# Performance work log

Measured on AMD Instinct MI355X. Metric: run time of the kernel, lower is better.

Reference implementation:

```python
import jax, jax.numpy as jnp
import numpy as np
import math

B, S, D, H, PD = 2, 2048, 1024, 16, 3
DK = D // H          # 64
SP = S // H          # 128, required so physics_scores matches scores shape


def setup_inputs() -> dict:
    key = jax.random.key(0)
    ks = jax.random.split(key, 16)
    sc = 0.02
    return {
        "query": jax.random.normal(ks[0], (B, S, D), jnp.float32),
        "key_in": jax.random.normal(ks[1], (B, S, D), jnp.float32),
        "value": jax.random.normal(ks[2], (B, S, D), jnp.float32),
        "physics_info": jax.random.normal(ks[3], (B, SP, PD), jnp.float32),
        "Wq": jax.random.normal(ks[4], (D, D), jnp.float32) * sc,
        "bq": jnp.zeros((D,), jnp.float32),
        "Wk": jax.random.normal(ks[5], (D, D), jnp.float32) * sc,
        "bk": jnp.zeros((D,), jnp.float32),
        "Wv": jax.random.normal(ks[6], (D, D), jnp.float32) * sc,
        "bv": jnp.zeros((D,), jnp.float32),
        "Wo": jax.random.normal(ks[7], (D, D), jnp.float32) * sc,
        "bo": jnp.zeros((D,), jnp.float32),
        "Pw": jax.random.normal(ks[8], (PD, D), jnp.float32),   # physics_weight
        "pb": jnp.zeros((1,), jnp.float32),                      # physics_bias
    }


def reference(query, key_in, value, physics_info, Wq, bq, Wk, bk, Wv, bv, Wo, bo, Pw, pb):
    b, s, d = query.shape
    inv = 1.0 / math.sqrt(DK)
    # project and split heads -> [B, H, S, DK]
    Q = (query @ Wq + bq).reshape(b, s, H, DK).transpose(0, 2, 1, 3)
    K = (key_in @ Wk + bk).reshape(b, s, H, DK).transpose(0, 2, 1, 3)
    V = (value @ Wv + bv).reshape(b, s, H, DK).transpose(0, 2, 1, 3)
    scores = jnp.einsum('bhqd,bhkd->bhqk', Q, K) * inv  # [B,H,S,S]
    # physics constraint: [B,SP,D] -> (expand over heads is a no-op) -> [B,SP*H,DK]
    pc = (physics_info @ Pw).reshape(b, SP * H, DK)
    physics_scores = jnp.einsum('bhqd,bkd->bhqk', Q, pc) * inv  # [B,H,S,S]
    scores = scores + pb[0] * physics_scores
    attn = jax.nn.softmax(scores, axis=-1)  # dropout in eval mode (identity)
    ctx = jnp.einsum('bhqk,bhkd->bhqd', attn, V)
    ctx = ctx.transpose(0, 2, 1, 3).reshape(b, s, d)
    return ctx @ Wo + bo
```

## Files before the change

### kernel.cpp

```cpp
#include <hip/hip_runtime.h>
#include <hip/hip_bf16.h>
#include <stdint.h>

typedef __bf16 bf16_t;
typedef __attribute__((ext_vector_type(8))) __bf16 bf16x8;
typedef __attribute__((ext_vector_type(4))) __bf16 bf16x4;
typedef __attribute__((ext_vector_type(4))) short short4_t;
typedef __attribute__((ext_vector_type(4))) float f32x4;

#define B_ 2
#define S_ 2048
#define D_ 1024
#define H_ 16
#define DK_ 64
#define SP_ 128

static __device__ inline f32x4 mfma16x16x16bf16(short4_t a, short4_t b, f32x4 c) {
#if __has_builtin(__builtin_amdgcn_mfma_f32_16x16x16bf16_1k)
    return __builtin_amdgcn_mfma_f32_16x16x16bf16_1k(a, b, c, 0, 0, 0);
#else
    asm volatile("v_mfma_f32_16x16x16_bf16 %0, %1, %2, %0" : "+v"(c) : "v"(a), "v"(b));
    return c;
#endif
}

__global__ __launch_bounds__(256) void physics_pc(const float* __restrict__ phys,
                                                  const float* __restrict__ Pw,
                                                  float* __restrict__ PP) {
    int i = blockIdx.x * 256 + threadIdx.x;
    int n = i & (D_ - 1);
    int sb = i >> 10;
    float acc = 0.f;
#pragma unroll
    for (int p = 0; p < 3; ++p)
        acc += phys[sb * 3 + p] * Pw[p * D_ + n];
    PP[i] = acc;
}

struct WPtrs { const float* w[4]; bf16_t* o[4]; };

__global__ __launch_bounds__(256) void wconv_t(WPtrs p) {
    __shared__ bf16_t t[32][33];
    int z = blockIdx.z;
    const float* W = p.w[z];
    bf16_t* Wt = p.o[z];
    int bx = blockIdx.x * 32, by = blockIdx.y * 32;
    int x = threadIdx.x, y0 = threadIdx.y;
#pragma unroll
    for (int j = 0; j < 32; j += 8)
        t[y0 + j][x] = (bf16_t)W[(size_t)(by + y0 + j) * D_ + bx + x];
    __syncthreads();
#pragma unroll
    for (int j = 0; j < 32; j += 8)
        Wt[(size_t)(bx + y0 + j) * D_ + by + x] = t[x][y0 + j];
}

__global__ __launch_bounds__(256) void qkv_gemm(
    const float* __restrict__ q_in, const float* __restrict__ k_in,
    const float* __restrict__ v_in,
    const bf16_t* __restrict__ WqT, const bf16_t* __restrict__ WkT,
    const bf16_t* __restrict__ WvT,
    const float* __restrict__ bq, const float* __restrict__ bk,
    const float* __restrict__ bv,
    bf16_t* __restrict__ Qo, bf16_t* __restrict__ Ko, bf16_t* __restrict__ Vo,
    const float* __restrict__ PP, const float* __restrict__ pbp) {
    __shared__ alignas(16) bf16_t lA[128 * 64];
    __shared__ alignas(16) bf16_t lB[128 * 64];
    int z = blockIdx.z;
    const float* A = (z == 0) ? q_in : (z == 1) ? k_in : v_in;
    const bf16_t* Bt = (z == 0) ? WqT : (z == 1) ? WkT : WvT;
    const float* bias = (z == 0) ? bq : (z == 1) ? bk : bv;

    int tid = threadIdx.x;
    int lane = tid & 63, wid = tid >> 6;
    int quad = lane >> 4, l15 = lane & 15;
    int bm = blockIdx.x * 128;
    int bn = blockIdx.y * 128;
    int wm = (wid >> 1) * 64, wn = (wid & 1) * 64;
    f32x4 acc[4][4] = {};

    for (int k0 = 0; k0 < D_; k0 += 64) {
        const float* gA = A + (size_t)bm * D_ + k0;
        const char* gB = (const char*)(Bt + (size_t)bn * D_ + k0);
        f32x4 a0[4], a1[4];
        bf16x8 vb[4];
#pragma unroll
        for (int j = 0; j < 4; ++j) {
            int flatB = j * 8192 + tid * 32;
            int row = flatB >> 8;
            int col = (flatB & 255) >> 2;
            const float* pA = gA + (size_t)row * D_ + col;
            a0[j] = *(const f32x4*)pA;
            a1[j] = *(const f32x4*)(pA + 4);
            int flat = j * 4096 + tid * 16;
            vb[j] = *(const bf16x8*)(gB + (size_t)(flat >> 7) * (D_ * 2) + (flat & 127));
        }
        __syncthreads();
#pragma unroll
        for (int j = 0; j < 4; ++j) {
            bf16x8 av;
#pragma unroll
            for (int e = 0; e < 4; ++e) { av[e] = (bf16_t)a0[j][e]; av[4 + e] = (bf16_t)a1[j][e]; }
            int flat = j * 4096 + tid * 16;
            *(bf16x8*)((char*)lA + flat) = av;
            *(bf16x8*)((char*)lB + flat) = vb[j];
        }
        __syncthreads();
#pragma unroll
        for (int ks = 0; ks < 2; ++ks) {
            bf16x8 af[4], bfr[4];
#pragma unroll
            for (int i = 0; i < 4; ++i) {
                af[i] = *(const bf16x8*)((const char*)lA + (wm + i * 16 + l15) * 128 + ks * 64 + quad * 16);
                bfr[i] = *(const bf16x8*)((const char*)lB + (wn + i * 16 + l15) * 128 + ks * 64 + quad * 16);
            }
#pragma unroll
            for (int i = 0; i < 4; ++i)
#pragma unroll
                for (int j = 0; j < 4; ++j)
                    acc[i][j] = __builtin_amdgcn_mfma_f32_16x16x32_bf16(af[i], bfr[j], acc[i][j], 0, 0, 0);
        }
    }

    float pb0 = (z == 1) ? pbp[0] : 0.f;
#pragma unroll
    for (int i = 0; i < 4; ++i)
#pragma unroll
        for (int j = 0; j < 4; ++j) {
            int r0 = bm + wm + i * 16 + quad * 4;
            int c = bn + wn + j * 16 + l15;
            float bv_ = bias[c];
#pragma unroll
            for (int reg = 0; reg < 4; ++reg) {
                int r = r0 + reg;
                float v = acc[i][j][reg] + bv_;
                if (z == 0) {
                    Qo[(size_t)r * D_ + c] = (bf16_t)(v * 0.125f);
                } else if (z == 1) {
                    int b = r >> 11, s = r & (S_ - 1);
                    v += pb0 * PP[((size_t)(b * SP_ + (s >> 4)) << 10) + ((s & 15) << 6) + (c & 63)];
                    Ko[(size_t)r * D_ + c] = (bf16_t)v;
                } else {
                    int b = r >> 11, s = r & (S_ - 1);
                    Vo[(((size_t)b << 10) + c) * S_ + s] = (bf16_t)v;
                }
            }
        }
}

#define KSTR 144
#define VSTR 272

__global__ __launch_bounds__(256) void flash_attn(const bf16_t* Qb,
                                                  const bf16_t* __restrict__ Kb,
                                                  const bf16_t* __restrict__ Vt,
                                                  bf16_t* Ctx) {
    __shared__ alignas(16) char lK[128 * KSTR];
    __shared__ alignas(16) char lV[64 * VSTR];
    int tid = threadIdx.x, lane = tid & 63, wid = tid >> 6;
    int quad = lane >> 4, l15 = lane & 15;
    int q0 = blockIdx.x * 128;
    int h = blockIdx.y, b = blockIdx.z;
    const bf16_t* Qh = Qb + ((size_t)b * S_) * D_ + h * DK_;
    const bf16_t* Kh = Kb + ((size_t)b * S_) * D_ + h * DK_;
    const bf16_t* Vh = Vt + ((size_t)b * D_ + h * DK_) * S_;

    {
        const char* g = (const char*)(Qh + (size_t)q0 * D_);
#pragma unroll
        for (int j = 0; j < 4; ++j) {
            int flat = j * 4096 + tid * 16;
            bf16x8 v = *(const bf16x8*)(g + (size_t)(flat >> 7) * (D_ * 2) + (flat & 127));
            *(bf16x8*)(lK + (flat >> 7) * KSTR + (flat & 127)) = v;
        }
    }
    __syncthreads();
    bf16x8 qf[2][2];
#pragma unroll
    for (int mt = 0; mt < 2; ++mt)
#pragma unroll
        for (int ks = 0; ks < 2; ++ks)
            qf[mt][ks] = *(const bf16x8*)(lK + (wid * 32 + mt * 16 + l15) * KSTR + ks * 64 + quad * 16);

    f32x4 ot[4][2] = {};
    float m_i[2], l_i[2];
#pragma unroll
    for (int mt = 0; mt < 2; ++mt) { m_i[mt] = -1e30f; l_i[mt] = 0.f; }

    for (int t = 0; t < S_ / 128; ++t) {
        const char* gK = (const char*)(Kh + (size_t)t * 128 * D_);
        const char* gV = (const char*)(Vh + (size_t)t * 128);
        bf16x8 vk[4], vv[4];
#pragma unroll
        for (int j = 0; j < 4; ++j) {
            int flat = j * 4096 + tid * 16;
            vk[j] = *(const bf16x8*)(gK + (size_t)(flat >> 7) * (D_ * 2) + (flat & 127));
            vv[j] = *(const bf16x8*)(gV + (size_t)(flat >> 8) * (S_ * 2) + (flat & 255));
        }
        __syncthreads();
#pragma unroll
        for (int j = 0; j < 4; ++j) {
            int flat = j * 4096 + tid * 16;
            *(bf16x8*)(lK + (flat >> 7) * KSTR + (flat & 127)) = vk[j];
            *(bf16x8*)(lV + (flat >> 8) * VSTR + (flat & 255)) = vv[j];
        }
        __syncthreads();

        f32x4 sc[8][2];
#pragma unroll
        for (int kt = 0; kt < 8; ++kt)
#pragma unroll
            for (int mt = 0; mt < 2; ++mt) sc[kt][mt] = (f32x4){0.f, 0.f, 0.f, 0.f};
#pragma unroll
        for (int kt = 0; kt < 8; ++kt) {
            bf16x8 kf0 = *(const bf16x8*)(lK + (kt * 16 + l15) * KSTR + quad * 16);
            bf16x8 kf1 = *(const bf16x8*)(lK + (kt * 16 + l15) * KSTR + 64 + quad * 16);
#pragma unroll
            for (int mt = 0; mt < 2; ++mt) {
                sc[kt][mt] = __builtin_amdgcn_mfma_f32_16x16x32_bf16(kf0, qf[mt][0], sc[kt][mt], 0, 0, 0);
                sc[kt][mt] = __builtin_amdgcn_mfma_f32_16x16x32_bf16(kf1, qf[mt][1], sc[kt][mt], 0, 0, 0);
            }
        }

#pragma unroll
        for (int mt = 0; mt < 2; ++mt) {
            float mloc = -1e30f;
#pragma unroll
            for (int kt = 0; kt < 8; ++kt)
#pragma unroll
                for (int r = 0; r < 4; ++r) mloc = fmaxf(mloc, sc[kt][mt][r]);
            mloc = fmaxf(mloc, __shfl_xor(mloc, 16, 64));
            mloc = fmaxf(mloc, __shfl_xor(mloc, 32, 64));
            float mnew = fmaxf(m_i[mt], mloc);
            float alpha = __expf(m_i[mt] - mnew);
            float rsum = 0.f;
#pragma unroll
            for (int kt = 0; kt < 8; ++kt)
#pragma unroll
                for (int r = 0; r < 4; ++r) {
                    float p = __expf(sc[kt][mt][r] - mnew);
                    sc[kt][mt][r] = p;
                    rsum += p;
                }
            rsum += __shfl_xor(rsum, 16, 64);
            rsum += __shfl_xor(rsum, 32, 64);
            l_i[mt] = l_i[mt] * alpha + rsum;
            m_i[mt] = mnew;
#pragma unroll
            for (int dt = 0; dt < 4; ++dt)
#pragma unroll
                for (int r = 0; r < 4; ++r) ot[dt][mt][r] *= alpha;
        }

#pragma unroll
        for (int kt = 0; kt < 8; ++kt) {
            short4_t bp[2];
#pragma unroll
            for (int mt = 0; mt < 2; ++mt) {
                bf16x4 t4;
#pragma unroll
                for (int r = 0; r < 4; ++r) t4[r] = (bf16_t)sc[kt][mt][r];
                bp[mt] = *(short4_t*)&t4;
            }
#pragma unroll
            for (int dt = 0; dt < 4; ++dt) {
                bf16x4 a4 = *(const bf16x4*)(lV + (dt * 16 + l15) * VSTR + kt * 32 + quad * 8);
                short4_t ap = *(short4_t*)&a4;
#pragma unroll
                for (int mt = 0; mt < 2; ++mt)
                    ot[dt][mt] = mfma16x16x16bf16(ap, bp[mt], ot[dt][mt]);
            }
        }
    }

    __syncthreads();
#pragma unroll
    for (int mt = 0; mt < 2; ++mt) {
        float inv_l = 1.0f / l_i[mt];
#pragma unroll
        for (int dt = 0; dt < 4; ++dt) {
            bf16x4 t4;
#pragma unroll
            for (int r = 0; r < 4; ++r) t4[r] = (bf16_t)(ot[dt][mt][r] * inv_l);
            *(bf16x4*)(lK + (wid * 32 + mt * 16 + l15) * KSTR + dt * 32 + quad * 8) = t4;
        }
    }
    __syncthreads();
    {
        char* gout = (char*)(Ctx + ((size_t)b * S_ + q0) * D_ + h * DK_);
#pragma unroll
        for (int j = 0; j < 4; ++j) {
            int flat = j * 4096 + tid * 16;
            bf16x8 v = *(const bf16x8*)(lK + (flat >> 7) * KSTR + (flat & 127));
            *(bf16x8*)(gout + (size_t)(flat >> 7) * (D_ * 2) + (flat & 127)) = v;
        }
    }
}

__global__ __launch_bounds__(256) void gemm_out(const bf16_t* __restrict__ A,
                                                const bf16_t* __restrict__ Bt,
                                                const float* __restrict__ bias,
                                                float* __restrict__ C) {
    __shared__ alignas(16) bf16_t lA[128 * 64];
    __shared__ alignas(16) bf16_t lB[128 * 64];
    int tid = threadIdx.x;
    int lane = tid & 63, wid = tid >> 6;
    int quad = lane >> 4, l15 = lane & 15;
    int bm = blockIdx.x * 128;
    int bn = blockIdx.y * 128;
    int wm = (wid >> 1) * 64, wn = (wid & 1) * 64;
    f32x4 acc[4][4] = {};

    for (int k0 = 0; k0 < D_; k0 += 64) {
        const char* gA = (const char*)(A + (size_t)bm * D_ + k0);
        const char* gB = (const char*)(Bt + (size_t)bn * D_ + k0);
        bf16x8 va[4], vb[4];
#pragma unroll
        for (int j = 0; j < 4; ++j) {
            int flat = j * 4096 + tid * 16;
            va[j] = *(const bf16x8*)(gA + (size_t)(flat >> 7) * (D_ * 2) + (flat & 127));
            vb[j] = *(const bf16x8*)(gB + (size_t)(flat >> 7) * (D_ * 2) + (flat & 127));
        }
        __syncthreads();
#pragma unroll
        for (int j = 0; j < 4; ++j) {
            int flat = j * 4096 + tid * 16;
            *(bf16x8*)((char*)lA + flat) = va[j];
            *(bf16x8*)((char*)lB + flat) = vb[j];
        }
        __syncthreads();
#pragma unroll
        for (int ks = 0; ks < 2; ++ks) {
            bf16x8 af[4], bfr[4];
#pragma unroll
            for (int i = 0; i < 4; ++i) {
                af[i] = *(const bf16x8*)((const char*)lA + (wm + i * 16 + l15) * 128 + ks * 64 + quad * 16);
                bfr[i] = *(const bf16x8*)((const char*)lB + (wn + i * 16 + l15) * 128 + ks * 64 + quad * 16);
            }
#pragma unroll
            for (int i = 0; i < 4; ++i)
#pragma unroll
                for (int j = 0; j < 4; ++j)
                    acc[i][j] = __builtin_amdgcn_mfma_f32_16x16x32_bf16(af[i], bfr[j], acc[i][j], 0, 0, 0);
        }
    }
#pragma unroll
    for (int i = 0; i < 4; ++i)
#pragma unroll
        for (int j = 0; j < 4; ++j) {
            int r0 = bm + wm + i * 16 + quad * 4;
            int c = bn + wn + j * 16 + l15;
            float bv_ = bias[c];
#pragma unroll
            for (int reg = 0; reg < 4; ++reg)
                C[(size_t)(r0 + reg) * D_ + c] = acc[i][j][reg] + bv_;
        }
}

extern "C" void kernel_launch(void* const* d_in, const int* in_sizes, int n_in,
                              void* d_out, int out_size, void* d_ws, size_t ws_size,
                              hipStream_t stream) {
    const float* query  = (const float*)d_in[0];
    const float* key_in = (const float*)d_in[1];
    const float* value  = (const float*)d_in[2];
    const float* phys   = (const float*)d_in[3];
    const float* Wq     = (const float*)d_in[4];
    const float* bq     = (const float*)d_in[5];
    const float* Wk     = (const float*)d_in[6];
    const float* bk     = (const float*)d_in[7];
    const float* Wv     = (const float*)d_in[8];
    const float* bv     = (const float*)d_in[9];
    const float* Wo     = (const float*)d_in[10];
    const float* bo     = (const float*)d_in[11];
    const float* Pw     = (const float*)d_in[12];
    const float* pb     = (const float*)d_in[13];

    char* ws = (char*)d_ws;
    const size_t MB = 1ull << 20;
    bf16_t* Kb  = (bf16_t*)(ws + 0 * MB);
    bf16_t* QC  = (bf16_t*)(ws + 8 * MB);
    bf16_t* WqT = (bf16_t*)(ws + 16 * MB);
    bf16_t* WkT = (bf16_t*)(ws + 18 * MB);
    bf16_t* WvT = (bf16_t*)(ws + 20 * MB);
    bf16_t* WoT = (bf16_t*)(ws + 22 * MB);
    float*  PP  = (float*)(ws + 24 * MB);
    bf16_t* Vt  = (bf16_t*)d_out;

    physics_pc<<<(B_ * SP_ * D_) / 256, 256, 0, stream>>>(phys, Pw, PP);

    WPtrs wp;
    wp.w[0] = Wq; wp.w[1] = Wk; wp.w[2] = Wv; wp.w[3] = Wo;
    wp.o[0] = WqT; wp.o[1] = WkT; wp.o[2] = WvT; wp.o[3] = WoT;
    wconv_t<<<dim3(32, 32, 4), dim3(32, 8), 0, stream>>>(wp);

    dim3 gq(32, 8, 3);
    qkv_gemm<<<gq, 256, 0, stream>>>(query, key_in, value, WqT, WkT, WvT,
                                     bq, bk, bv, QC, Kb, Vt, PP, pb);

    dim3 fg(S_ / 128, H_, B_);
    flash_attn<<<fg, 256, 0, stream>>>(QC, Kb, Vt, QC);

    dim3 gg(32, 8);
    gemm_out<<<gg, 256, 0, stream>>>(QC, WoT, bo, (float*)d_out);
}
```

Baseline: 278.4 us.

## Pre-convert QKV inputs to bf16 and stage GEMM tiles via global_load_lds

Adds a separate conversion kernel that casts query, key and value from fp32 to bf16 into workspace and d_out scratch. The QKV and output GEMMs then load bf16 tiles directly into LDS with global_load_lds instead of staging through registers. The aim is to cut register pressure and VGPR-to-LDS copy work in the GEMM main loops. In exchange it adds an extra pass over the inputs, writing and rereading 24 MB of bf16. It also places Qin inside the output buffer, which needs care to avoid overlapping Vt.

```diff
diff --git a/kernel.cpp b/kernel.cpp
--- a/kernel.cpp
+++ b/kernel.cpp
@@ -7,6 +7,9 @@
 typedef __attribute__((ext_vector_type(4))) __bf16 bf16x4;
 typedef __attribute__((ext_vector_type(4))) short short4_t;
 typedef __attribute__((ext_vector_type(4))) float f32x4;
+
+#define GLOBAL_AS(p) ((const __attribute__((address_space(1))) void*)(p))
+#define LDS_AS(p)    ((__attribute__((address_space(3))) void*)(p))
 
 #define B_ 2
 #define S_ 2048
@@ -24,6 +27,24 @@
 #endif
 }
 
+__global__ __launch_bounds__(256) void conv3(const float* __restrict__ q,
+                                             const float* __restrict__ k,
+                                             const float* __restrict__ v,
+                                             bf16_t* __restrict__ qo,
+                                             bf16_t* __restrict__ ko,
+                                             bf16_t* __restrict__ vo) {
+    int z = blockIdx.y;
+    const float* in = (z == 0) ? q : (z == 1) ? k : v;
+    bf16_t* out = (z == 0) ? qo : (z == 1) ? ko : vo;
+    size_t i = ((size_t)blockIdx.x * 256 + threadIdx.x) * 8;
+    f32x4 a = *(const f32x4*)(in + i);
+    f32x4 b = *(const f32x4*)(in + i + 4);
+    bf16x8 o;
+#pragma unroll
+    for (int e = 0; e < 4; ++e) { o[e] = (bf16_t)a[e]; o[4 + e] = (bf16_t)b[e]; }
+    *(bf16x8*)(out + i) = o;
+}
+
 __global__ __launch_bounds__(256) void physics_pc(const float* __restrict__ phys,
                                                   const float* __restrict__ Pw,
                                                   float* __restrict__ PP) {
@@ -56,8 +77,8 @@
 }
 
 __global__ __launch_bounds__(256) void qkv_gemm(
-    const float* __restrict__ q_in, const float* __restrict__ k_in,
-    const float* __restrict__ v_in,
+    const bf16_t* __restrict__ Qi, const bf16_t* __restrict__ Ki,
+    const bf16_t* __restrict__ Vi,
     const bf16_t* __restrict__ WqT, const bf16_t* __restrict__ WkT,
     const bf16_t* __restrict__ WvT,
     const float* __restrict__ bq, const float* __restrict__ bk,
@@ -67,7 +88,7 @@
     __shared__ alignas(16) bf16_t lA[128 * 64];
     __shared__ alignas(16) bf16_t lB[128 * 64];
     int z = blockIdx.z;
-    const float* A = (z == 0) ? q_in : (z == 1) ? k_in : v_in;
+    const bf16_t* A = (z == 0) ? Qi : (z == 1) ? Ki : Vi;
     const bf16_t* Bt = (z == 0) ? WqT : (z == 1) ? WkT : WvT;
     const float* bias = (z == 0) ? bq : (z == 1) ? bk : bv;
 
@@ -80,30 +101,18 @@
     f32x4 acc[4][4] = {};
 
     for (int k0 = 0; k0 < D_; k0 += 64) {
-        const float* gA = A + (size_t)bm * D_ + k0;
+        __syncthreads();
+        const char* gA = (const char*)(A + (size_t)bm * D_ + k0);
         const char* gB = (const char*)(Bt + (size_t)bn * D_ + k0);
-        f32x4 a0[4], a1[4];
-        bf16x8 vb[4];
-#pragma unroll
-        for (int j = 0; j < 4; ++j) {
-            int flatB = j * 8192 + tid * 32;
-            int row = flatB >> 8;
-            int col = (flatB & 255) >> 2;
-            const float* pA = gA + (size_t)row * D_ + col;
-            a0[j] = *(const f32x4*)pA;
-            a1[j] = *(const f32x4*)(pA + 4);
-            int flat = j * 4096 + tid * 16;
-            vb[j] = *(const bf16x8*)(gB + (size_t)(flat >> 7) * (D_ * 2) + (flat & 127));
-        }
-        __syncthreads();
-#pragma unroll
-        for (int j = 0; j < 4; ++j) {
-            bf16x8 av;
-#pragma unroll
-            for (int e = 0; e < 4; ++e) { av[e] = (bf16_t)a0[j][e]; av[4 + e] = (bf16_t)a1[j][e]; }
-            int flat = j * 4096 + tid * 16;
-            *(bf16x8*)((char*)lA + flat) = av;
-            *(bf16x8*)((char*)lB + flat) = vb[j];
+#pragma unroll
+        for (int j = 0; j < 4; ++j) {
+            int woff = j * 4096 + wid * 1024;
+            int fl = woff + lane * 16;
+            int row = fl >> 7, col = fl & 127;
+            __builtin_amdgcn_global_load_lds(GLOBAL_AS(gA + (size_t)row * (D_ * 2) + col),
+                                             LDS_AS((char*)lA + woff), 16, 0, 0);
+            __builtin_amdgcn_global_load_lds(GLOBAL_AS(gB + (size_t)row * (D_ * 2) + col),
+                                             LDS_AS((char*)lB + woff), 16, 0, 0);
         }
         __syncthreads();
 #pragma unroll
@@ -312,21 +321,18 @@
     f32x4 acc[4][4] = {};
 
     for (int k0 = 0; k0 < D_; k0 += 64) {
+        __syncthreads();
         const char* gA = (const char*)(A + (size_t)bm * D_ + k0);
         const char* gB = (const char*)(Bt + (size_t)bn * D_ + k0);
-        bf16x8 va[4], vb[4];
-#pragma unroll
-        for (int j = 0; j < 4; ++j) {
-            int flat = j * 4096 + tid * 16;
-            va[j] = *(const bf16x8*)(gA + (size_t)(flat >> 7) * (D_ * 2) + (flat & 127));
-            vb[j] = *(const bf16x8*)(gB + (size_t)(flat >> 7) * (D_ * 2) + (flat & 127));
-        }
-        __syncthreads();
-#pragma unroll
-        for (int j = 0; j < 4; ++j) {
-            int flat = j * 4096 + tid * 16;
-            *(bf16x8*)((char*)lA + flat) = va[j];
-            *(bf16x8*)((char*)lB + flat) = vb[j];
+#pragma unroll
+        for (int j = 0; j < 4; ++j) {
+            int woff = j * 4096 + wid * 1024;
+            int fl = woff + lane * 16;
+            int row = fl >> 7, col = fl & 127;
+            __builtin_amdgcn_global_load_lds(GLOBAL_AS(gA + (size_t)row * (D_ * 2) + col),
+                                             LDS_AS((char*)lA + woff), 16, 0, 0);
+            __builtin_amdgcn_global_load_lds(GLOBAL_AS(gB + (size_t)row * (D_ * 2) + col),
+                                             LDS_AS((char*)lB + woff), 16, 0, 0);
         }
         __syncthreads();
 #pragma unroll
@@ -379,22 +385,28 @@
     const size_t MB = 1ull << 20;
     bf16_t* Kb  = (bf16_t*)(ws + 0 * MB);
     bf16_t* QC  = (bf16_t*)(ws + 8 * MB);
-    bf16_t* WqT = (bf16_t*)(ws + 16 * MB);
-    bf16_t* WkT = (bf16_t*)(ws + 18 * MB);
-    bf16_t* WvT = (bf16_t*)(ws + 20 * MB);
-    bf16_t* WoT = (bf16_t*)(ws + 22 * MB);
-    float*  PP  = (float*)(ws + 24 * MB);
+    bf16_t* Kin = (bf16_t*)(ws + 16 * MB);
+    bf16_t* Vin = (bf16_t*)(ws + 24 * MB);
+    bf16_t* WqT = (bf16_t*)(ws + 32 * MB);
+    bf16_t* WkT = (bf16_t*)(ws + 34 * MB);
+    bf16_t* WvT = (bf16_t*)(ws + 36 * MB);
+    bf16_t* WoT = (bf16_t*)(ws + 38 * MB);
+    float*  PP  = (float*)(ws + 40 * MB);
     bf16_t* Vt  = (bf16_t*)d_out;
-
-    physics_pc<<<(B_ * SP_ * D_) / 256, 256, 0, stream>>>(phys, Pw, PP);
+    bf16_t* Qin = (bf16_t*)((char*)d_out + 8 * MB);
+
+    conv3<<<dim3((B_ * S_ * D_) / (256 * 8), 3), 256, 0, stream>>>(
+        query, key_in, value, Qin, Kin, Vin);
 
     WPtrs wp;
     wp.w[0] = Wq; wp.w[1] = Wk; wp.w[2] = Wv; wp.w[3] = Wo;
     wp.o[0] = WqT; wp.o[1] = WkT; wp.o[2] = WvT; wp.o[3] = WoT;
     wconv_t<<<dim3(32, 32, 4), dim3(32, 8), 0, stream>>>(wp);
 
+    physics_pc<<<(B_ * SP_ * D_) / 256, 256, 0, stream>>>(phys, Pw, PP);
+
     dim3 gq(32, 8, 3);
-    qkv_gemm<<<gq, 256, 0, stream>>>(query, key_in, value, WqT, WkT, WvT,
+    qkv_gemm<<<gq, 256, 0, stream>>>(Qin, Kin, Vin, WqT, WkT, WvT,
                                      bq, bk, bv, QC, Kb, Vt, PP, pb);
 
     dim3 fg(S_ / 128, H_, B_);
```

Measured after the change: 272.6 us. -2.1%, faster.
